# Kernel tuning notes

Measured on AMD Instinct MI355X. Metric: run time of the kernel, lower is better.

The kernel has to match this reference:

```python
import jax, jax.numpy as jnp
import numpy as np

EPS = 1e-10
LN_EPS = 1e-5
WIN = 64          # entropy_window_size
STRIDE = WIN // 2 # 32
CDF_POINTS = 64   # entropy_cdf_points
D_MODEL = 256
STATS_DIM = 256 + 1 + CDF_POINTS  # 321
HID = 2 * D_MODEL  # 512


def setup_inputs() -> dict:
    key = jax.random.key(0)
    ks = jax.random.split(key, 8)
    B, L = 64, 65536
    x = jax.random.randint(ks[0], (B, L), 0, 256)

    def lin(k, fan_in, fan_out):
        return jax.random.normal(k, (fan_in, fan_out), jnp.float32) * (1.0 / np.sqrt(fan_in))

    return {
        "x": x,
        "W1": lin(ks[1], STATS_DIM, HID), "b1": jnp.zeros((HID,), jnp.float32),
        "g1": jnp.ones((HID,), jnp.float32), "be1": jnp.zeros((HID,), jnp.float32),
        "W2": lin(ks[2], HID, HID), "b2": jnp.zeros((HID,), jnp.float32),
        "g2": jnp.ones((HID,), jnp.float32), "be2": jnp.zeros((HID,), jnp.float32),
        "W3": lin(ks[3], HID, D_MODEL), "b3": jnp.zeros((D_MODEL,), jnp.float32),
    }


def _entropy(counts):
    # Shannon entropy (bits) over last axis; matches torch compute_entropy.
    total = counts.sum(axis=-1, keepdims=True)
    probs = counts / (total + EPS)
    return -(probs * jnp.log2(probs + EPS)).sum(axis=-1)


def _layernorm(h, g, b):
    mu = h.mean(axis=-1, keepdims=True)
    var = ((h - mu) ** 2).mean(axis=-1, keepdims=True)
    return (h - mu) * jax.lax.rsqrt(var + LN_EPS) * g + b


def reference(x, W1, b1, g1, be1, W2, b2, g2, be2, W3, b3):
    B, L = x.shape
    xb = jnp.clip(x, 0, 255)

    # Global byte histogram via scatter-add (no one-hot materialization).
    hist = jnp.zeros((B, 256), jnp.float32).at[jnp.arange(B)[:, None], xb].add(1.0)
    normalized_hist = hist / (jnp.float32(L) + EPS)
    global_entropy = _entropy(hist)[:, None]  # [B,1]

    nw = (L - WIN) // STRIDE + 1
    widx = jnp.arange(nw)[:, None] * STRIDE + jnp.arange(WIN)[None, :]
    wins = xb[:, widx].reshape(B * nw, WIN)
    rows = jnp.arange(B * nw)[:, None]
    whist = jnp.zeros((B * nw, 256), jnp.float32).at[rows, wins].add(1.0)
    went = _entropy(whist).reshape(B, nw)  # [B, nw]

    # Empirical CDF of window entropies at linspace(0,8,CDF_POINTS).
    levels = jnp.linspace(0.0, 8.0, CDF_POINTS)
    cdf = (went[:, :, None] <= levels[None, None, :]).astype(jnp.float32).mean(axis=1)

    feats = jnp.concatenate([normalized_hist, global_entropy, cdf], axis=1)  # [B, 321]

    # Projector MLP (dropout omitted: eval mode).
    h = _layernorm(feats @ W1 + b1, g1, be1)
    h = jax.nn.relu(h)
    h = _layernorm(h @ W2 + b2, g2, be2)
    h = jax.nn.relu(h)
    return h @ W3 + b3  # [B, d_model]
```

## Files before the change

### kernel.cpp

```cpp
#include <hip/hip_runtime.h>

#define BATCH 64
#define LLEN 65536
#define NW 2047
#define STATS 321
#define NCHUNK 32

__device__ __forceinline__ float dppWaveSumBcast(float x) {
    float t;
    t = __int_as_float(__builtin_amdgcn_update_dpp(0, __float_as_int(x), 0x111, 0xf, 0xf, true));  x += t;
    t = __int_as_float(__builtin_amdgcn_update_dpp(0, __float_as_int(x), 0x112, 0xf, 0xf, true));  x += t;
    t = __int_as_float(__builtin_amdgcn_update_dpp(0, __float_as_int(x), 0x114, 0xf, 0xf, true));  x += t;
    t = __int_as_float(__builtin_amdgcn_update_dpp(0, __float_as_int(x), 0x118, 0xf, 0xf, true));  x += t;
    t = __int_as_float(__builtin_amdgcn_update_dpp(0, __float_as_int(x), 0x142, 0xa, 0xf, false)); x += t;
    t = __int_as_float(__builtin_amdgcn_update_dpp(0, __float_as_int(x), 0x143, 0xc, 0xf, false)); x += t;
    return __int_as_float(__builtin_amdgcn_readlane(__float_as_int(x), 63));
}

__global__ __launch_bounds__(256) void front_kernel(const int* __restrict__ x,
                                                    int* __restrict__ hpart,
                                                    int* __restrict__ cpart) {
    __shared__ int lh[256];
    __shared__ int lc[256];
    const int row = blockIdx.y;
    const int c = blockIdx.x;
    const int t = threadIdx.x;
    const int lane = t & 63;
    const int wave = t >> 6;
    lh[t] = 0;
    __syncthreads();

    const int* xr = x + row * LLEN;
    const int eb = c * 2048 + wave * 512;

    int e[9];
#pragma unroll
    for (int j = 0; j < 8; ++j) e[j] = min(max(xr[eb + j * 64 + lane], 0), 255);
    e[8] = min(max(xr[min(eb + 512, LLEN - 64) + lane], 0), 255);

    const float lv = (lane == 63) ? 8.0f : (float)lane * (8.0f / 63.0f);
    const float T = (6.0f - lv) * 64.0f;
    const int wbase = c * 64 + wave * 16;
    const int xlane = lane ^ 32;

    unsigned Blo[8], Bhi[8];
#pragma unroll
    for (int k = 0; k < 8; ++k) {
        const unsigned long long b = __ballot(e[0] & (1 << k));
        Blo[k] = (unsigned)b;
        Bhi[k] = (unsigned)(b >> 32);
    }

    int cnt = 0;
#pragma unroll
    for (int j = 0; j < 8; ++j) {
        unsigned Nlo[8], Nhi[8];
#pragma unroll
        for (int k = 0; k < 8; ++k) {
            const unsigned long long b = __ballot(e[j + 1] & (1 << k));
            Nlo[k] = (unsigned)b;
            Nhi[k] = (unsigned)(b >> 32);
        }
        const int srcv = (lane < 32) ? e[j + 1] : e[j];
        const int u = __shfl(srcv, xlane);

        {
            unsigned mlo = 0xffffffffu, mhi = 0xffffffffu;
#pragma unroll
            for (int k = 0; k < 8; ++k) {
                const unsigned s = (unsigned)(((e[j] >> k) & 1) - 1);
                mlo &= Blo[k] ^ s;
                mhi &= Bhi[k] ^ s;
            }
            const int cc = __popc(mlo) + __popc(mhi);
            const float S = dppWaveSumBcast(__log2f((float)cc));
            cnt += (int)(S >= T);
            unsigned below = __builtin_amdgcn_mbcnt_lo(mlo, 0u);
            below = __builtin_amdgcn_mbcnt_hi(mhi, below);
            if (below == 0u) atomicAdd(&lh[e[j]], cc);
        }

        {
            unsigned mlo = 0xffffffffu, mhi = 0xffffffffu;
#pragma unroll
            for (int k = 0; k < 8; ++k) {
                const unsigned s = (unsigned)(((u >> k) & 1) - 1);
                mlo &= Bhi[k] ^ s;
                mhi &= Nlo[k] ^ s;
            }
            const int cc = __popc(mlo) + __popc(mhi);
            const float S = dppWaveSumBcast(__log2f((float)cc));
            cnt += (int)((S >= T) && (wbase + 2 * j + 1 < NW));
        }

#pragma unroll
        for (int k = 0; k < 8; ++k) { Blo[k] = Nlo[k]; Bhi[k] = Nhi[k]; }
    }
    lc[t] = cnt;
    __syncthreads();

    hpart[(row * NCHUNK + c) * 256 + t] = lh[t];
    if (t < 64)
        cpart[(row * NCHUNK + c) * 64 + t] = lc[t] + lc[64 + t] + lc[128 + t] + lc[192 + t];
}

__global__ __launch_bounds__(256) void gemm1_kernel(
    const int* __restrict__ hpart, const int* __restrict__ cpart,
    const float* __restrict__ W, const float* __restrict__ b,
    float* __restrict__ out) {
    __shared__ float sa[STATS];
    __shared__ float red[4];
    __shared__ float part[16][64];
    const int row = blockIdx.y;
    const int t = threadIdx.x;

    int h = 0;
    const int* hp = hpart + row * (NCHUNK * 256) + t;
#pragma unroll
    for (int ch = 0; ch < NCHUNK; ++ch) h += hp[ch * 256];
    const float p = (float)h * (1.0f / 65536.0f);
    sa[t] = p;
    const float term = -p * log2f(p + 1e-10f);
    const float s = dppWaveSumBcast(term);
    if ((t & 63) == 0) red[t >> 6] = s;

    if (t < 64) {
        int cc = 0;
        const int* cp = cpart + row * (NCHUNK * 64) + t;
#pragma unroll
        for (int ch = 0; ch < NCHUNK; ++ch) cc += cp[ch * 64];
        sa[257 + t] = (float)cc * (1.0f / 2047.0f);
    }
    __syncthreads();
    if (t == 0) sa[256] = red[0] + red[1] + red[2] + red[3];
    __syncthreads();

    const int cl = (t & 15) * 4;
    const int col = blockIdx.x * 64 + cl;
    const int kg = t >> 4;
    const int klo = kg * 21;
    const int khi = min(klo + 21, STATS);
    float4 acc = {0.f, 0.f, 0.f, 0.f};
    for (int k = klo; k < khi; ++k) {
        const float a = sa[k];
        const float4 w = *(const float4*)&W[k * 512 + col];
        acc.x = fmaf(a, w.x, acc.x);
        acc.y = fmaf(a, w.y, acc.y);
        acc.z = fmaf(a, w.z, acc.z);
        acc.w = fmaf(a, w.w, acc.w);
    }
    *(float4*)&part[kg][cl] = acc;
    __syncthreads();
    if (t < 64) {
        float o = b[blockIdx.x * 64 + t];
#pragma unroll
        for (int g = 0; g < 16; ++g) o += part[g][t];
        out[row * 512 + blockIdx.x * 64 + t] = o;
    }
}

template <int NOUT, int CPB>
__global__ __launch_bounds__(256) void gemm_ln_kernel(
    const float* __restrict__ raw, const float* __restrict__ g,
    const float* __restrict__ be, const float* __restrict__ W,
    const float* __restrict__ b, float* __restrict__ out) {
    constexpr int TC = CPB / 4;
    constexpr int KG = 256 / TC;
    constexpr int KI = 512 / KG;
    __shared__ float sa[512];
    __shared__ float red[8];
    __shared__ float part[KG][CPB];
    const int row = blockIdx.y;
    const int t = threadIdx.x;

    const float v1 = raw[row * 512 + t];
    const float v2 = raw[row * 512 + 256 + t];
    const float s = dppWaveSumBcast(v1 + v2);
    const float q = dppWaveSumBcast(v1 * v1 + v2 * v2);
    if ((t & 63) == 0) { red[t >> 6] = s; red[4 + (t >> 6)] = q; }
    __syncthreads();
    const float mu = (red[0] + red[1] + red[2] + red[3]) * (1.0f / 512.0f);
    const float var = (red[4] + red[5] + red[6] + red[7]) * (1.0f / 512.0f) - mu * mu;
    const float rs = rsqrtf(var + 1e-5f);
    sa[t] = fmaxf((v1 - mu) * rs * g[t] + be[t], 0.0f);
    sa[t + 256] = fmaxf((v2 - mu) * rs * g[t + 256] + be[t + 256], 0.0f);
    __syncthreads();

    const int cl = (t % TC) * 4;
    const int col = blockIdx.x * CPB + cl;
    const int kg = t / TC;
    float4 acc = {0.f, 0.f, 0.f, 0.f};
#pragma unroll
    for (int i = 0; i < KI; ++i) {
        const int k = kg * KI + i;
        const float a = sa[k];
        const float4 w = *(const float4*)&W[k * NOUT + col];
        acc.x = fmaf(a, w.x, acc.x);
        acc.y = fmaf(a, w.y, acc.y);
        acc.z = fmaf(a, w.z, acc.z);
        acc.w = fmaf(a, w.w, acc.w);
    }
    *(float4*)&part[kg][cl] = acc;
    __syncthreads();
    if (t < CPB) {
        float o = b[blockIdx.x * CPB + t];
#pragma unroll
        for (int gi = 0; gi < KG; ++gi) o += part[gi][t];
        out[row * NOUT + blockIdx.x * CPB + t] = o;
    }
}

extern "C" void kernel_launch(void* const* d_in, const int* in_sizes, int n_in,
                              void* d_out, int out_size, void* d_ws, size_t ws_size,
                              hipStream_t stream) {
    const int* x = (const int*)d_in[0];
    const float* W1 = (const float*)d_in[1];
    const float* b1 = (const float*)d_in[2];
    const float* g1 = (const float*)d_in[3];
    const float* be1 = (const float*)d_in[4];
    const float* W2 = (const float*)d_in[5];
    const float* b2 = (const float*)d_in[6];
    const float* g2 = (const float*)d_in[7];
    const float* be2 = (const float*)d_in[8];
    const float* W3 = (const float*)d_in[9];
    const float* b3 = (const float*)d_in[10];
    float* out = (float*)d_out;

    char* ws = (char*)d_ws;
    int* hpart = (int*)ws;
    int* cpart = (int*)(ws + 2097152);
    float* raw1 = (float*)(ws + 2621440);
    float* raw2 = (float*)(ws + 2752512);

    front_kernel<<<dim3(NCHUNK, BATCH), 256, 0, stream>>>(x, hpart, cpart);
    gemm1_kernel<<<dim3(8, BATCH), 256, 0, stream>>>(hpart, cpart, W1, b1, raw1);
    gemm_ln_kernel<512, 64><<<dim3(8, BATCH), 256, 0, stream>>>(raw1, g1, be1, W2, b2, raw2);
    gemm_ln_kernel<256, 32><<<dim3(8, BATCH), 256, 0, stream>>>(raw2, g2, be2, W3, b3, out);
}
```

Baseline: 113.1 us.

## Reduce front partials with global atomics and batch four rows per MLP block

```diff
diff --git a/kernel.cpp b/kernel.cpp
--- a/kernel.cpp
+++ b/kernel.cpp
@@ -18,8 +18,8 @@
 }
 
 __global__ __launch_bounds__(256) void front_kernel(const int* __restrict__ x,
-                                                    int* __restrict__ hpart,
-                                                    int* __restrict__ cpart) {
+                                                    int* __restrict__ hist,
+                                                    int* __restrict__ ccnt) {
     __shared__ int lh[256];
     __shared__ int lc[256];
     const int row = blockIdx.y;
@@ -99,114 +99,158 @@
     lc[t] = cnt;
     __syncthreads();
 
-    hpart[(row * NCHUNK + c) * 256 + t] = lh[t];
+    atomicAdd(&hist[row * 256 + t], lh[t]);
     if (t < 64)
-        cpart[(row * NCHUNK + c) * 64 + t] = lc[t] + lc[64 + t] + lc[128 + t] + lc[192 + t];
+        atomicAdd(&ccnt[row * 64 + t], lc[t] + lc[64 + t] + lc[128 + t] + lc[192 + t]);
 }
 
 __global__ __launch_bounds__(256) void gemm1_kernel(
-    const int* __restrict__ hpart, const int* __restrict__ cpart,
+    const int* __restrict__ hist, const int* __restrict__ ccnt,
     const float* __restrict__ W, const float* __restrict__ b,
     float* __restrict__ out) {
-    __shared__ float sa[STATS];
-    __shared__ float red[4];
-    __shared__ float part[16][64];
-    const int row = blockIdx.y;
+    __shared__ float feats[4][324];
+    __shared__ float reds[4][4];
+    __shared__ float part[4][4][64];
     const int t = threadIdx.x;
-
-    int h = 0;
-    const int* hp = hpart + row * (NCHUNK * 256) + t;
-#pragma unroll
-    for (int ch = 0; ch < NCHUNK; ++ch) h += hp[ch * 256];
-    const float p = (float)h * (1.0f / 65536.0f);
-    sa[t] = p;
-    const float term = -p * log2f(p + 1e-10f);
-    const float s = dppWaveSumBcast(term);
-    if ((t & 63) == 0) red[t >> 6] = s;
-
-    if (t < 64) {
-        int cc = 0;
-        const int* cp = cpart + row * (NCHUNK * 64) + t;
-#pragma unroll
-        for (int ch = 0; ch < NCHUNK; ++ch) cc += cp[ch * 64];
-        sa[257 + t] = (float)cc * (1.0f / 2047.0f);
-    }
-    __syncthreads();
-    if (t == 0) sa[256] = red[0] + red[1] + red[2] + red[3];
-    __syncthreads();
-
-    const int cl = (t & 15) * 4;
-    const int col = blockIdx.x * 64 + cl;
-    const int kg = t >> 4;
-    const int klo = kg * 21;
-    const int khi = min(klo + 21, STATS);
-    float4 acc = {0.f, 0.f, 0.f, 0.f};
-    for (int k = klo; k < khi; ++k) {
-        const float a = sa[k];
-        const float4 w = *(const float4*)&W[k * 512 + col];
-        acc.x = fmaf(a, w.x, acc.x);
-        acc.y = fmaf(a, w.y, acc.y);
-        acc.z = fmaf(a, w.z, acc.z);
-        acc.w = fmaf(a, w.w, acc.w);
-    }
-    *(float4*)&part[kg][cl] = acc;
-    __syncthreads();
-    if (t < 64) {
-        float o = b[blockIdx.x * 64 + t];
-#pragma unroll
-        for (int g = 0; g < 16; ++g) o += part[g][t];
-        out[row * 512 + blockIdx.x * 64 + t] = o;
-    }
-}
-
-template <int NOUT, int CPB>
+    const int lane = t & 63;
+    const int wave = t >> 6;
+    const int rb = blockIdx.y * 4;
+
+#pragma unroll
+    for (int r = 0; r < 4; ++r) {
+        const int h = hist[(rb + r) * 256 + t];
+        const float p = (float)h * (1.0f / 65536.0f);
+        feats[r][t] = p;
+        const float term = -p * log2f(p + 1e-10f);
+        const float s = dppWaveSumBcast(term);
+        if (lane == 0) reds[r][wave] = s;
+    }
+    {
+        const int r = t >> 6, lv = t & 63;
+        feats[r][257 + lv] = (float)ccnt[(rb + r) * 64 + lv] * (1.0f / 2047.0f);
+    }
+    __syncthreads();
+    if (t < 4) feats[t][256] = reds[t][0] + reds[t][1] + reds[t][2] + reds[t][3];
+    __syncthreads();
+
+    const int colbase = blockIdx.x * 64;
+    const float* Wc = W + colbase + lane;
+    float acc0 = 0.f, acc1 = 0.f, acc2 = 0.f, acc3 = 0.f;
+    const int klo = wave * 84;
+    const int khi = min(klo + 84, STATS);
+    int k = klo;
+    for (; k + 4 <= khi; k += 4) {
+        const float4 a0 = *(const float4*)&feats[0][k];
+        const float4 a1 = *(const float4*)&feats[1][k];
+        const float4 a2 = *(const float4*)&feats[2][k];
+        const float4 a3 = *(const float4*)&feats[3][k];
+        const float w0 = Wc[(k + 0) * 512];
+        const float w1 = Wc[(k + 1) * 512];
+        const float w2 = Wc[(k + 2) * 512];
+        const float w3 = Wc[(k + 3) * 512];
+        acc0 = fmaf(a0.x, w0, acc0); acc0 = fmaf(a0.y, w1, acc0);
+        acc0 = fmaf(a0.z, w2, acc0); acc0 = fmaf(a0.w, w3, acc0);
+        acc1 = fmaf(a1.x, w0, acc1); acc1 = fmaf(a1.y, w1, acc1);
+        acc1 = fmaf(a1.z, w2, acc1); acc1 = fmaf(a1.w, w3, acc1);
+        acc2 = fmaf(a2.x, w0, acc2); acc2 = fmaf(a2.y, w1, acc2);
+        acc2 = fmaf(a2.z, w2, acc2); acc2 = fmaf(a2.w, w3, acc2);
+        acc3 = fmaf(a3.x, w0, acc3); acc3 = fmaf(a3.y, w1, acc3);
+        acc3 = fmaf(a3.z, w2, acc3); acc3 = fmaf(a3.w, w3, acc3);
+    }
+    for (; k < khi; ++k) {
+        const float w = Wc[k * 512];
+        acc0 = fmaf(feats[0][k], w, acc0);
+        acc1 = fmaf(feats[1][k], w, acc1);
+        acc2 = fmaf(feats[2][k], w, acc2);
+        acc3 = fmaf(feats[3][k], w, acc3);
+    }
+    part[wave][0][lane] = acc0;
+    part[wave][1][lane] = acc1;
+    part[wave][2][lane] = acc2;
+    part[wave][3][lane] = acc3;
+    __syncthreads();
+    {
+        const int r2 = t >> 6, c2 = t & 63;
+        float o = b[colbase + c2];
+#pragma unroll
+        for (int gI = 0; gI < 4; ++gI) o += part[gI][r2][c2];
+        out[(rb + r2) * 512 + colbase + c2] = o;
+    }
+}
+
+template <int NOUT, int COLS>
 __global__ __launch_bounds__(256) void gemm_ln_kernel(
     const float* __restrict__ raw, const float* __restrict__ g,
     const float* __restrict__ be, const float* __restrict__ W,
     const float* __restrict__ b, float* __restrict__ out) {
-    constexpr int TC = CPB / 4;
-    constexpr int KG = 256 / TC;
+    constexpr int KG = 256 / COLS;
     constexpr int KI = 512 / KG;
-    __shared__ float sa[512];
-    __shared__ float red[8];
-    __shared__ float part[KG][CPB];
-    const int row = blockIdx.y;
+    __shared__ float sa[4][512];
+    __shared__ float reds[4][4];
+    __shared__ float redq[4][4];
+    __shared__ float part[KG][4][COLS];
     const int t = threadIdx.x;
-
-    const float v1 = raw[row * 512 + t];
-    const float v2 = raw[row * 512 + 256 + t];
-    const float s = dppWaveSumBcast(v1 + v2);
-    const float q = dppWaveSumBcast(v1 * v1 + v2 * v2);
-    if ((t & 63) == 0) { red[t >> 6] = s; red[4 + (t >> 6)] = q; }
-    __syncthreads();
-    const float mu = (red[0] + red[1] + red[2] + red[3]) * (1.0f / 512.0f);
-    const float var = (red[4] + red[5] + red[6] + red[7]) * (1.0f / 512.0f) - mu * mu;
-    const float rs = rsqrtf(var + 1e-5f);
-    sa[t] = fmaxf((v1 - mu) * rs * g[t] + be[t], 0.0f);
-    sa[t + 256] = fmaxf((v2 - mu) * rs * g[t + 256] + be[t + 256], 0.0f);
-    __syncthreads();
-
-    const int cl = (t % TC) * 4;
-    const int col = blockIdx.x * CPB + cl;
-    const int kg = t / TC;
-    float4 acc = {0.f, 0.f, 0.f, 0.f};
-#pragma unroll
-    for (int i = 0; i < KI; ++i) {
-        const int k = kg * KI + i;
-        const float a = sa[k];
-        const float4 w = *(const float4*)&W[k * NOUT + col];
-        acc.x = fmaf(a, w.x, acc.x);
-        acc.y = fmaf(a, w.y, acc.y);
-        acc.z = fmaf(a, w.z, acc.z);
-        acc.w = fmaf(a, w.w, acc.w);
-    }
-    *(float4*)&part[kg][cl] = acc;
-    __syncthreads();
-    if (t < CPB) {
-        float o = b[blockIdx.x * CPB + t];
-#pragma unroll
-        for (int gi = 0; gi < KG; ++gi) o += part[gi][t];
-        out[row * NOUT + blockIdx.x * CPB + t] = o;
+    const int lane = t & 63;
+    const int wave = t >> 6;
+    const int rb = blockIdx.y * 4;
+
+    const float gv1 = g[t], gv2 = g[t + 256];
+    const float bv1 = be[t], bv2 = be[t + 256];
+    float vr1[4], vr2[4];
+#pragma unroll
+    for (int r = 0; r < 4; ++r) {
+        vr1[r] = raw[(rb + r) * 512 + t];
+        vr2[r] = raw[(rb + r) * 512 + 256 + t];
+        const float s = dppWaveSumBcast(vr1[r] + vr2[r]);
+        const float q = dppWaveSumBcast(vr1[r] * vr1[r] + vr2[r] * vr2[r]);
+        if (lane == 0) { reds[r][wave] = s; redq[r][wave] = q; }
+    }
+    __syncthreads();
+#pragma unroll
+    for (int r = 0; r < 4; ++r) {
+        const float mu = (reds[r][0] + reds[r][1] + reds[r][2] + reds[r][3]) * (1.0f / 512.0f);
+        const float var = (redq[r][0] + redq[r][1] + redq[r][2] + redq[r][3]) * (1.0f / 512.0f) - mu * mu;
+        const float rs = rsqrtf(var + 1e-5f);
+        sa[r][t] = fmaxf((vr1[r] - mu) * rs * gv1 + bv1, 0.0f);
+        sa[r][t + 256] = fmaxf((vr2[r] - mu) * rs * gv2 + bv2, 0.0f);
+    }
+    __syncthreads();
+
+    const int col = t % COLS;
+    const int kg = t / COLS;
+    const int colbase = blockIdx.x * COLS;
+    const float* Wc = W + colbase + col;
+    float acc0 = 0.f, acc1 = 0.f, acc2 = 0.f, acc3 = 0.f;
+    const int klo = kg * KI;
+    for (int k = klo; k < klo + KI; k += 4) {
+        const float4 a0 = *(const float4*)&sa[0][k];
+        const float4 a1 = *(const float4*)&sa[1][k];
+        const float4 a2 = *(const float4*)&sa[2][k];
+        const float4 a3 = *(const float4*)&sa[3][k];
+        const float w0 = Wc[(k + 0) * NOUT];
+        const float w1 = Wc[(k + 1) * NOUT];
+        const float w2 = Wc[(k + 2) * NOUT];
+        const float w3 = Wc[(k + 3) * NOUT];
+        acc0 = fmaf(a0.x, w0, acc0); acc0 = fmaf(a0.y, w1, acc0);
+        acc0 = fmaf(a0.z, w2, acc0); acc0 = fmaf(a0.w, w3, acc0);
+        acc1 = fmaf(a1.x, w0, acc1); acc1 = fmaf(a1.y, w1, acc1);
+        acc1 = fmaf(a1.z, w2, acc1); acc1 = fmaf(a1.w, w3, acc1);
+        acc2 = fmaf(a2.x, w0, acc2); acc2 = fmaf(a2.y, w1, acc2);
+        acc2 = fmaf(a2.z, w2, acc2); acc2 = fmaf(a2.w, w3, acc2);
+        acc3 = fmaf(a3.x, w0, acc3); acc3 = fmaf(a3.y, w1, acc3);
+        acc3 = fmaf(a3.z, w2, acc3); acc3 = fmaf(a3.w, w3, acc3);
+    }
+    part[kg][0][col] = acc0;
+    part[kg][1][col] = acc1;
+    part[kg][2][col] = acc2;
+    part[kg][3][col] = acc3;
+    __syncthreads();
+    if (t < 4 * COLS) {
+        const int r2 = t / COLS, c2 = t % COLS;
+        float o = b[colbase + c2];
+#pragma unroll
+        for (int gI = 0; gI < KG; ++gI) o += part[gI][r2][c2];
+        out[(rb + r2) * NOUT + colbase + c2] = o;
     }
 }
 
@@ -227,13 +271,14 @@
     float* out = (float*)d_out;
 
     char* ws = (char*)d_ws;
-    int* hpart = (int*)ws;
-    int* cpart = (int*)(ws + 2097152);
-    float* raw1 = (float*)(ws + 2621440);
-    float* raw2 = (float*)(ws + 2752512);
-
-    front_kernel<<<dim3(NCHUNK, BATCH), 256, 0, stream>>>(x, hpart, cpart);
-    gemm1_kernel<<<dim3(8, BATCH), 256, 0, stream>>>(hpart, cpart, W1, b1, raw1);
-    gemm_ln_kernel<512, 64><<<dim3(8, BATCH), 256, 0, stream>>>(raw1, g1, be1, W2, b2, raw2);
-    gemm_ln_kernel<256, 32><<<dim3(8, BATCH), 256, 0, stream>>>(raw2, g2, be2, W3, b3, out);
-}
+    int* hist = (int*)ws;
+    int* ccnt = (int*)(ws + 65536);
+    float* raw1 = (float*)(ws + 81920);
+    float* raw2 = (float*)(ws + 212992);
+
+    hipMemsetAsync(ws, 0, 81920, stream);
+    front_kernel<<<dim3(NCHUNK, BATCH), 256, 0, stream>>>(x, hist, ccnt);
+    gemm1_kernel<<<dim3(8, 16), 256, 0, stream>>>(hist, ccnt, W1, b1, raw1);
+    gemm_ln_kernel<512, 64><<<dim3(8, 16), 256, 0, stream>>>(raw1, g1, be1, W2, b2, raw2);
+    gemm_ln_kernel<256, 32><<<dim3(8, 16), 256, 0, stream>>>(raw2, g2, be2, W3, b3, out);
+}
```

Result: no change. 113.8 us (+0.7%).

## Fuse three MLP GEMM/LayerNorm kernels into one per-row kernel

Applied to the files above, without the earlier changes.

```diff
diff --git a/kernel.cpp b/kernel.cpp
--- a/kernel.cpp
+++ b/kernel.cpp
@@ -79,7 +79,6 @@
             below = __builtin_amdgcn_mbcnt_hi(mhi, below);
             if (below == 0u) atomicAdd(&lh[e[j]], cc);
         }
-
         {
             unsigned mlo = 0xffffffffu, mhi = 0xffffffffu;
 #pragma unroll
@@ -92,7 +91,6 @@
             const float S = dppWaveSumBcast(__log2f((float)cc));
             cnt += (int)((S >= T) && (wbase + 2 * j + 1 < NW));
         }
-
 #pragma unroll
         for (int k = 0; k < 8; ++k) { Blo[k] = Nlo[k]; Bhi[k] = Nhi[k]; }
     }
@@ -104,110 +102,145 @@
         cpart[(row * NCHUNK + c) * 64 + t] = lc[t] + lc[64 + t] + lc[128 + t] + lc[192 + t];
 }
 
-__global__ __launch_bounds__(256) void gemm1_kernel(
+__global__ __launch_bounds__(512) void mlp_kernel(
     const int* __restrict__ hpart, const int* __restrict__ cpart,
-    const float* __restrict__ W, const float* __restrict__ b,
+    const float* __restrict__ W1, const float* __restrict__ b1,
+    const float* __restrict__ g1, const float* __restrict__ be1,
+    const float* __restrict__ W2, const float* __restrict__ b2,
+    const float* __restrict__ g2, const float* __restrict__ be2,
+    const float* __restrict__ W3, const float* __restrict__ b3,
     float* __restrict__ out) {
-    __shared__ float sa[STATS];
-    __shared__ float red[4];
-    __shared__ float part[16][64];
-    const int row = blockIdx.y;
+    __shared__ __align__(16) float feats[324];
+    __shared__ __align__(16) float sa[512];
+    __shared__ __align__(16) float p3[512];
+    __shared__ float red[8], redq[8];
+    const int row = blockIdx.x;
     const int t = threadIdx.x;
-
-    int h = 0;
-    const int* hp = hpart + row * (NCHUNK * 256) + t;
-#pragma unroll
-    for (int ch = 0; ch < NCHUNK; ++ch) h += hp[ch * 256];
-    const float p = (float)h * (1.0f / 65536.0f);
-    sa[t] = p;
-    const float term = -p * log2f(p + 1e-10f);
-    const float s = dppWaveSumBcast(term);
-    if ((t & 63) == 0) red[t >> 6] = s;
-
-    if (t < 64) {
+    const int lane = t & 63;
+    const int wave = t >> 6;
+
+    if (t < 256) {
+        int h = 0;
+        const int* hp = hpart + row * (NCHUNK * 256) + t;
+#pragma unroll
+        for (int ch = 0; ch < NCHUNK; ++ch) h += hp[ch * 256];
+        const float p = (float)h * (1.0f / 65536.0f);
+        feats[t] = p;
+        const float term = -p * log2f(p + 1e-10f);
+        const float s = dppWaveSumBcast(term);
+        if (lane == 0) red[wave] = s;
+    } else if (t < 320) {
+        const int lv = t - 256;
         int cc = 0;
-        const int* cp = cpart + row * (NCHUNK * 64) + t;
+        const int* cp = cpart + row * (NCHUNK * 64) + lv;
 #pragma unroll
         for (int ch = 0; ch < NCHUNK; ++ch) cc += cp[ch * 64];
-        sa[257 + t] = (float)cc * (1.0f / 2047.0f);
-    }
-    __syncthreads();
-    if (t == 0) sa[256] = red[0] + red[1] + red[2] + red[3];
-    __syncthreads();
-
-    const int cl = (t & 15) * 4;
-    const int col = blockIdx.x * 64 + cl;
-    const int kg = t >> 4;
-    const int klo = kg * 21;
-    const int khi = min(klo + 21, STATS);
-    float4 acc = {0.f, 0.f, 0.f, 0.f};
-    for (int k = klo; k < khi; ++k) {
-        const float a = sa[k];
-        const float4 w = *(const float4*)&W[k * 512 + col];
-        acc.x = fmaf(a, w.x, acc.x);
-        acc.y = fmaf(a, w.y, acc.y);
-        acc.z = fmaf(a, w.z, acc.z);
-        acc.w = fmaf(a, w.w, acc.w);
-    }
-    *(float4*)&part[kg][cl] = acc;
-    __syncthreads();
-    if (t < 64) {
-        float o = b[blockIdx.x * 64 + t];
-#pragma unroll
-        for (int g = 0; g < 16; ++g) o += part[g][t];
-        out[row * 512 + blockIdx.x * 64 + t] = o;
-    }
-}
-
-template <int NOUT, int CPB>
-__global__ __launch_bounds__(256) void gemm_ln_kernel(
-    const float* __restrict__ raw, const float* __restrict__ g,
-    const float* __restrict__ be, const float* __restrict__ W,
-    const float* __restrict__ b, float* __restrict__ out) {
-    constexpr int TC = CPB / 4;
-    constexpr int KG = 256 / TC;
-    constexpr int KI = 512 / KG;
-    __shared__ float sa[512];
-    __shared__ float red[8];
-    __shared__ float part[KG][CPB];
-    const int row = blockIdx.y;
-    const int t = threadIdx.x;
-
-    const float v1 = raw[row * 512 + t];
-    const float v2 = raw[row * 512 + 256 + t];
-    const float s = dppWaveSumBcast(v1 + v2);
-    const float q = dppWaveSumBcast(v1 * v1 + v2 * v2);
-    if ((t & 63) == 0) { red[t >> 6] = s; red[4 + (t >> 6)] = q; }
-    __syncthreads();
-    const float mu = (red[0] + red[1] + red[2] + red[3]) * (1.0f / 512.0f);
-    const float var = (red[4] + red[5] + red[6] + red[7]) * (1.0f / 512.0f) - mu * mu;
-    const float rs = rsqrtf(var + 1e-5f);
-    sa[t] = fmaxf((v1 - mu) * rs * g[t] + be[t], 0.0f);
-    sa[t + 256] = fmaxf((v2 - mu) * rs * g[t + 256] + be[t + 256], 0.0f);
-    __syncthreads();
-
-    const int cl = (t % TC) * 4;
-    const int col = blockIdx.x * CPB + cl;
-    const int kg = t / TC;
-    float4 acc = {0.f, 0.f, 0.f, 0.f};
-#pragma unroll
-    for (int i = 0; i < KI; ++i) {
-        const int k = kg * KI + i;
-        const float a = sa[k];
-        const float4 w = *(const float4*)&W[k * NOUT + col];
-        acc.x = fmaf(a, w.x, acc.x);
-        acc.y = fmaf(a, w.y, acc.y);
-        acc.z = fmaf(a, w.z, acc.z);
-        acc.w = fmaf(a, w.w, acc.w);
-    }
-    *(float4*)&part[kg][cl] = acc;
-    __syncthreads();
-    if (t < CPB) {
-        float o = b[blockIdx.x * CPB + t];
-#pragma unroll
-        for (int gi = 0; gi < KG; ++gi) o += part[gi][t];
-        out[row * NOUT + blockIdx.x * CPB + t] = o;
-    }
+        feats[257 + lv] = (float)cc * (1.0f / 2047.0f);
+    }
+    __syncthreads();
+    if (t == 0) feats[256] = red[0] + red[1] + red[2] + red[3];
+    __syncthreads();
+
+    float raw;
+    {
+        float acc0 = 0.f, acc1 = 0.f;
+        const float* Wc = W1 + t;
+        int k = 0;
+        for (; k + 8 <= STATS; k += 8) {
+            const float4 a0 = *(const float4*)&feats[k];
+            const float4 a1 = *(const float4*)&feats[k + 4];
+            const float w0 = Wc[(k + 0) * 512];
+            const float w1 = Wc[(k + 1) * 512];
+            const float w2 = Wc[(k + 2) * 512];
+            const float w3 = Wc[(k + 3) * 512];
+            const float w4 = Wc[(k + 4) * 512];
+            const float w5 = Wc[(k + 5) * 512];
+            const float w6 = Wc[(k + 6) * 512];
+            const float w7 = Wc[(k + 7) * 512];
+            acc0 = fmaf(a0.x, w0, acc0); acc1 = fmaf(a0.y, w1, acc1);
+            acc0 = fmaf(a0.z, w2, acc0); acc1 = fmaf(a0.w, w3, acc1);
+            acc0 = fmaf(a1.x, w4, acc0); acc1 = fmaf(a1.y, w5, acc1);
+            acc0 = fmaf(a1.z, w6, acc0); acc1 = fmaf(a1.w, w7, acc1);
+        }
+        for (; k < STATS; ++k) acc0 = fmaf(feats[k], Wc[k * 512], acc0);
+        raw = acc0 + acc1 + b1[t];
+    }
+    {
+        const float s = dppWaveSumBcast(raw);
+        const float q = dppWaveSumBcast(raw * raw);
+        if (lane == 0) { red[wave] = s; redq[wave] = q; }
+        __syncthreads();
+        float ms = 0.f, qs = 0.f;
+#pragma unroll
+        for (int i = 0; i < 8; ++i) { ms += red[i]; qs += redq[i]; }
+        const float mu = ms * (1.0f / 512.0f);
+        const float var = qs * (1.0f / 512.0f) - mu * mu;
+        const float rs = rsqrtf(var + 1e-5f);
+        sa[t] = fmaxf((raw - mu) * rs * g1[t] + be1[t], 0.0f);
+        __syncthreads();
+    }
+    {
+        float acc0 = 0.f, acc1 = 0.f;
+        const float* Wc = W2 + t;
+#pragma unroll 4
+        for (int k = 0; k < 512; k += 8) {
+            const float4 a0 = *(const float4*)&sa[k];
+            const float4 a1 = *(const float4*)&sa[k + 4];
+            const float w0 = Wc[(k + 0) * 512];
+            const float w1 = Wc[(k + 1) * 512];
+            const float w2 = Wc[(k + 2) * 512];
+            const float w3 = Wc[(k + 3) * 512];
+            const float w4 = Wc[(k + 4) * 512];
+            const float w5 = Wc[(k + 5) * 512];
+            const float w6 = Wc[(k + 6) * 512];
+            const float w7 = Wc[(k + 7) * 512];
+            acc0 = fmaf(a0.x, w0, acc0); acc1 = fmaf(a0.y, w1, acc1);
+            acc0 = fmaf(a0.z, w2, acc0); acc1 = fmaf(a0.w, w3, acc1);
+            acc0 = fmaf(a1.x, w4, acc0); acc1 = fmaf(a1.y, w5, acc1);
+            acc0 = fmaf(a1.z, w6, acc0); acc1 = fmaf(a1.w, w7, acc1);
+        }
+        raw = acc0 + acc1 + b2[t];
+    }
+    {
+        const float s = dppWaveSumBcast(raw);
+        const float q = dppWaveSumBcast(raw * raw);
+        if (lane == 0) { red[wave] = s; redq[wave] = q; }
+        __syncthreads();
+        float ms = 0.f, qs = 0.f;
+#pragma unroll
+        for (int i = 0; i < 8; ++i) { ms += red[i]; qs += redq[i]; }
+        const float mu = ms * (1.0f / 512.0f);
+        const float var = qs * (1.0f / 512.0f) - mu * mu;
+        const float rs = rsqrtf(var + 1e-5f);
+        sa[t] = fmaxf((raw - mu) * rs * g2[t] + be2[t], 0.0f);
+        __syncthreads();
+    }
+    {
+        const int c = t & 255;
+        const int k0 = (t >> 8) << 8;
+        float acc0 = 0.f, acc1 = 0.f;
+        const float* Wc = W3 + c;
+#pragma unroll 4
+        for (int k = k0; k < k0 + 256; k += 8) {
+            const float4 a0 = *(const float4*)&sa[k];
+            const float4 a1 = *(const float4*)&sa[k + 4];
+            const float w0 = Wc[(k + 0) * 256];
+            const float w1 = Wc[(k + 1) * 256];
+            const float w2 = Wc[(k + 2) * 256];
+            const float w3 = Wc[(k + 3) * 256];
+            const float w4 = Wc[(k + 4) * 256];
+            const float w5 = Wc[(k + 5) * 256];
+            const float w6 = Wc[(k + 6) * 256];
+            const float w7 = Wc[(k + 7) * 256];
+            acc0 = fmaf(a0.x, w0, acc0); acc1 = fmaf(a0.y, w1, acc1);
+            acc0 = fmaf(a0.z, w2, acc0); acc1 = fmaf(a0.w, w3, acc1);
+            acc0 = fmaf(a1.x, w4, acc0); acc1 = fmaf(a1.y, w5, acc1);
+            acc0 = fmaf(a1.z, w6, acc0); acc1 = fmaf(a1.w, w7, acc1);
+        }
+        p3[t] = acc0 + acc1;
+    }
+    __syncthreads();
+    if (t < 256) out[row * 256 + t] = b3[t] + p3[t] + p3[256 + t];
 }
 
 extern "C" void kernel_launch(void* const* d_in, const int* in_sizes, int n_in,
@@ -229,11 +262,10 @@
     char* ws = (char*)d_ws;
     int* hpart = (int*)ws;
     int* cpart = (int*)(ws + 2097152);
-    float* raw1 = (float*)(ws + 2621440);
-    float* raw2 = (float*)(ws + 2752512);
 
     front_kernel<<<dim3(NCHUNK, BATCH), 256, 0, stream>>>(x, hpart, cpart);
-    gemm1_kernel<<<dim3(8, BATCH), 256, 0, stream>>>(hpart, cpart, W1, b1, raw1);
-    gemm_ln_kernel<512, 64><<<dim3(8, BATCH), 256, 0, stream>>>(raw1, g1, be1, W2, b2, raw2);
-    gemm_ln_kernel<256, 32><<<dim3(8, BATCH), 256, 0, stream>>>(raw2, g2, be2, W3, b3, out);
-}
+    mlp_kernel<<<dim3(BATCH), 512, 0, stream>>>(hpart, cpart,
+                                                W1, b1, g1, be1,
+                                                W2, b2, g2, be2,
+                                                W3, b3, out);
+}
```

Result: no change. 114.7 us (+1.4%).
